# Kernel optimization log

Hardware: AMD Instinct MI355X
Metric: run time of the kernel (lower is better)

Reference implementation:

```python
import jax, jax.numpy as jnp
import numpy as np

N = 50000   # nodes
E = 800000  # edges
IN, H, OUT = 64, 512, 128


def _lin_init(key, out_dim, in_dim):
    kw, kb = jax.random.split(key)
    bound = 1.0 / np.sqrt(in_dim)
    W = jax.random.uniform(kw, (out_dim, in_dim), jnp.float32, -bound, bound)
    b = jax.random.uniform(kb, (out_dim,), jnp.float32, -bound, bound)
    return W, b


def setup_inputs() -> dict:
    key = jax.random.key(0)
    ks = jax.random.split(key, 10)
    x = jax.random.normal(ks[0], (N, IN), jnp.float32)
    edge_index = jax.random.randint(ks[1], (2, E), 0, N, jnp.int64)
    W_s1, b_s1 = _lin_init(ks[2], H, IN)
    W_s2, b_s2 = _lin_init(ks[3], H, H)
    W_s3, b_s3 = _lin_init(ks[4], H, H)
    W_s4, b_s4 = _lin_init(ks[5], H, H)
    W_m1, b_m1 = _lin_init(ks[6], OUT, H)
    W_m2, b_m2 = _lin_init(ks[7], OUT, OUT)
    W_l1, b_l1 = _lin_init(ks[8], OUT, H)
    W_l2, b_l2 = _lin_init(ks[9], OUT, OUT)
    return {"x": x, "edge_index": edge_index,
            "W_s1": W_s1, "b_s1": b_s1, "W_s2": W_s2, "b_s2": b_s2,
            "W_s3": W_s3, "b_s3": b_s3, "W_s4": W_s4, "b_s4": b_s4,
            "W_m1": W_m1, "b_m1": b_m1, "W_m2": W_m2, "b_m2": b_m2,
            "W_l1": W_l1, "b_l1": b_l1, "W_l2": W_l2, "b_l2": b_l2}


def _aggregate(h, src, dst):
    # GINConv with default eps=0: (1+eps)*x + sum_{j in N(i)} x_j
    return h + jax.ops.segment_sum(h[src], dst, num_segments=N)


def reference(x, edge_index,
              W_s1, b_s1, W_s2, b_s2, W_s3, b_s3, W_s4, b_s4,
              W_m1, b_m1, W_m2, b_m2, W_l1, b_l1, W_l2, b_l2):
    src, dst = edge_index[0], edge_index[1]
    lrelu = lambda v: jax.nn.leaky_relu(v, 0.1)

    def mlp_shared(h):
        h = lrelu(h @ W_s1.T + b_s1)
        h = lrelu(h @ W_s2.T + b_s2)
        h = lrelu(h @ W_s3.T + b_s3)
        return h @ W_s4.T + b_s4

    def mlp_mu(h):
        return jax.nn.relu(h @ W_m1.T + b_m1) @ W_m2.T + b_m2

    def mlp_logvar(h):
        return jax.nn.relu(h @ W_l1.T + b_l1) @ W_l2.T + b_l2

    h = jax.nn.relu(mlp_shared(_aggregate(x, src, dst)))
    mu = mlp_mu(_aggregate(h, src, dst))
    logvar = mlp_logvar(_aggregate(h, src, dst))
    return (mu, logvar)
```

## Files before the change

kernel.cpp:

```cpp
#include <hip/hip_runtime.h>
#include <hip/hip_bf16.h>
#include <stdint.h>

#define N_NODES 50000
#define N_PAD   50048
#define E_EDGES 800000
#define MT      391

typedef __bf16 bf16x8 __attribute__((ext_vector_type(8)));
typedef __bf16 bf16x4 __attribute__((ext_vector_type(4)));
typedef float  f32x4  __attribute__((ext_vector_type(4)));

__global__ void count_deg(const int* __restrict__ ei, int* __restrict__ cnt) {
    int e = blockIdx.x * blockDim.x + threadIdx.x;
    if (e < E_EDGES) atomicAdd(&cnt[ei[E_EDGES + e]], 1);
}

#define SCAN_B 1024
__global__ void scan_block(const int* __restrict__ cnt, int* __restrict__ ptr,
                           int* __restrict__ bsum, int n) {
    __shared__ int buf[SCAN_B];
    int i = blockIdx.x * SCAN_B + threadIdx.x;
    int v = (i < n) ? cnt[i] : 0;
    buf[threadIdx.x] = v;
    __syncthreads();
    #pragma unroll
    for (int off = 1; off < SCAN_B; off <<= 1) {
        int t = (threadIdx.x >= (unsigned)off) ? buf[threadIdx.x - off] : 0;
        __syncthreads();
        buf[threadIdx.x] += t;
        __syncthreads();
    }
    if (i < n) ptr[i] = buf[threadIdx.x] - v;
    if (threadIdx.x == SCAN_B - 1) bsum[blockIdx.x] = buf[SCAN_B - 1];
}

__global__ void scan_bsums(const int* __restrict__ bsum, int* __restrict__ boff,
                           int nb, int* __restrict__ total_out) {
    __shared__ int buf[SCAN_B];
    int v = ((int)threadIdx.x < nb) ? bsum[threadIdx.x] : 0;
    buf[threadIdx.x] = v;
    __syncthreads();
    #pragma unroll
    for (int off = 1; off < SCAN_B; off <<= 1) {
        int t = (threadIdx.x >= (unsigned)off) ? buf[threadIdx.x - off] : 0;
        __syncthreads();
        buf[threadIdx.x] += t;
        __syncthreads();
    }
    if ((int)threadIdx.x < nb) boff[threadIdx.x] = buf[threadIdx.x] - v;
    if (threadIdx.x == SCAN_B - 1) *total_out = buf[SCAN_B - 1];
}

__global__ void scan_add(int* __restrict__ ptr, const int* __restrict__ boff, int n) {
    int i = blockIdx.x * SCAN_B + threadIdx.x;
    if (i < n) ptr[i] += boff[blockIdx.x];
}

__global__ void fill_csr(const int* __restrict__ ei, const int* __restrict__ ptr,
                         int* __restrict__ cursor, int* __restrict__ col) {
    int e = blockIdx.x * blockDim.x + threadIdx.x;
    if (e < E_EDGES) {
        int dst = ei[E_EDGES + e];
        int pos = ptr[dst] + atomicAdd(&cursor[dst], 1);
        col[pos] = ei[e];
    }
}

#define XN      3200000
#define WTOT    983040
__global__ void cvt_all(const float* __restrict__ x,
                        const float* __restrict__ Ws1, const float* __restrict__ Ws2,
                        const float* __restrict__ Ws3, const float* __restrict__ Ws4,
                        const float* __restrict__ Wm1, const float* __restrict__ Wl1,
                        const float* __restrict__ Wm2, const float* __restrict__ Wl2,
                        __bf16* __restrict__ xb, __bf16* __restrict__ wbuf) {
    int i = blockIdx.x * blockDim.x + threadIdx.x;
    if (i < XN) { xb[i] = (__bf16)x[i]; return; }
    int j = i - XN;
    if (j >= WTOT) return;
    const float* s; int o;
    if      (j <  32768) { s = Ws1; o = j; }
    else if (j < 294912) { s = Ws2; o = j -  32768; }
    else if (j < 557056) { s = Ws3; o = j - 294912; }
    else if (j < 819200) { s = Ws4; o = j - 557056; }
    else if (j < 884736) { s = Wm1; o = j - 819200; }
    else if (j < 950272) { s = Wl1; o = j - 884736; }
    else if (j < 966656) { s = Wm2; o = j - 950272; }
    else                 { s = Wl2; o = j - 966656; }
    wbuf[j] = (__bf16)s[o];
}

__global__ __launch_bounds__(256) void agg0_gather(
    const __bf16* __restrict__ xb, const int* __restrict__ ptr,
    const int* __restrict__ col, __bf16* __restrict__ out) {
    int node = blockIdx.x * 4 + (threadIdx.x >> 6);
    int lane = threadIdx.x & 63;
    int g    = lane >> 3;
    int f0   = (lane & 7) << 3;
    if (node >= N_PAD) return;
    long o = (long)node * 64 + f0;
    if (node >= N_NODES) {
        if (g == 0) {
            bf16x8 z;
            #pragma unroll
            for (int i = 0; i < 8; ++i) z[i] = (__bf16)0.0f;
            *(bf16x8*)&out[o] = z;
        }
        return;
    }
    float a[8];
    #pragma unroll
    for (int i = 0; i < 8; ++i) a[i] = 0.0f;
    if (g == 0) {
        bf16x8 s = *(const bf16x8*)&xb[o];
        #pragma unroll
        for (int i = 0; i < 8; ++i) a[i] = (float)s[i];
    }
    int e0 = ptr[node], e1 = ptr[node + 1];
    int e = e0;
    for (; e + 16 <= e1; e += 16) {
        int c0 = col[e + g];
        int c1 = col[e + 8 + g];
        bf16x8 v0 = *(const bf16x8*)&xb[(c0 << 6) + f0];
        bf16x8 v1 = *(const bf16x8*)&xb[(c1 << 6) + f0];
        #pragma unroll
        for (int i = 0; i < 8; ++i) a[i] += (float)v0[i] + (float)v1[i];
    }
    int rem = e1 - e;
    if (rem > 0) {
        int u0 = (g < rem) ? g : 0;        float m0 = (g < rem) ? 1.0f : 0.0f;
        int i1 = g + 8;
        int u1 = (i1 < rem) ? i1 : 0;      float m1 = (i1 < rem) ? 1.0f : 0.0f;
        int c0 = col[e + u0];
        int c1 = col[e + u1];
        bf16x8 v0 = *(const bf16x8*)&xb[(c0 << 6) + f0];
        bf16x8 v1 = *(const bf16x8*)&xb[(c1 << 6) + f0];
        #pragma unroll
        for (int i = 0; i < 8; ++i) a[i] += m0 * (float)v0[i] + m1 * (float)v1[i];
    }
    #pragma unroll
    for (int i = 0; i < 8; ++i) {
        a[i] += __shfl_xor(a[i], 8, 64);
        a[i] += __shfl_xor(a[i], 16, 64);
        a[i] += __shfl_xor(a[i], 32, 64);
    }
    if (g == 0) {
        bf16x8 r;
        #pragma unroll
        for (int i = 0; i < 8; ++i) r[i] = (__bf16)a[i];
        *(bf16x8*)&out[o] = r;
    }
}

__global__ __launch_bounds__(256) void aggt_gather(
    const __bf16* __restrict__ t, const int* __restrict__ ptr,
    const int* __restrict__ col, const float* __restrict__ b_m1,
    const float* __restrict__ b_l1, __bf16* __restrict__ p) {
    int node = blockIdx.x * 8 + (threadIdx.x >> 5);
    if (node >= N_NODES) return;
    int hl = threadIdx.x & 31;
    int f0 = hl << 3;
    float a[8];
    {
        bf16x8 s = *(const bf16x8*)&t[((long)node << 8) + f0];
        #pragma unroll
        for (int i = 0; i < 8; ++i) a[i] = (float)s[i];
    }
    int e0 = ptr[node], e1 = ptr[node + 1];
    int e = e0;
    for (; e + 8 <= e1; e += 8) {
        int c[8];
        #pragma unroll
        for (int u = 0; u < 8; ++u) c[u] = col[e + u];
        bf16x8 v[8];
        #pragma unroll
        for (int u = 0; u < 8; ++u) v[u] = *(const bf16x8*)&t[((long)c[u] << 8) + f0];
        #pragma unroll
        for (int u = 0; u < 8; ++u)
            #pragma unroll
            for (int i = 0; i < 8; ++i) a[i] += (float)v[u][i];
    }
    int rem = e1 - e;
    if (rem > 0) {
        #pragma unroll
        for (int u = 0; u < 7; ++u) {
            int   uu = (u < rem) ? u : 0;
            float m  = (u < rem) ? 1.0f : 0.0f;
            int   cc = col[e + uu];
            bf16x8 v = *(const bf16x8*)&t[((long)cc << 8) + f0];
            #pragma unroll
            for (int i = 0; i < 8; ++i) a[i] += m * (float)v[i];
        }
    }
    const float* bp = (f0 < 128) ? (b_m1 + f0) : (b_l1 + (f0 - 128));
    f32x4 b0 = *(const f32x4*)bp;
    f32x4 b1 = *(const f32x4*)(bp + 4);
    bf16x8 r;
    #pragma unroll
    for (int i = 0; i < 4; ++i) r[i]     = (__bf16)fmaxf(a[i]     + b0[i], 0.0f);
    #pragma unroll
    for (int i = 0; i < 4; ++i) r[4 + i] = (__bf16)fmaxf(a[4 + i] + b1[i], 0.0f);
    *(bf16x8*)&p[((long)node << 8) + f0] = r;
}

__device__ __forceinline__ void gl_lds16(const __bf16* g, __bf16* l) {
    __builtin_amdgcn_global_load_lds(
        (const __attribute__((address_space(1))) uint32_t*)g,
        (__attribute__((address_space(3))) uint32_t*)l, 16, 0, 0);
}

#define P_WAITN(n) asm volatile("s_waitcnt vmcnt(" #n ")" ::: "memory")
#define P_WAIT0    asm volatile("s_waitcnt vmcnt(0)" ::: "memory")
#define P_LGKM0    asm volatile("s_waitcnt lgkmcnt(0)" ::: "memory")
#define P_BAR      __builtin_amdgcn_s_barrier()
#define SLOT_ELEMS 16384

__device__ __forceinline__ void stage_chunk(const __bf16* __restrict__ W, int Kdim,
                                            int k0, bool rows512,
                                            __bf16* __restrict__ buf,
                                            int wid, int lane) {
    if (rows512) {
        int r16 = lane >> 2, sl = lane & 3;
        #pragma unroll
        for (int i = 0; i < 4; ++i) {
            int cc = wid * 4 + i;
            int r  = cc * 16 + r16;
            int kt = sl ^ ((r >> 1) & 3);
            gl_lds16(W + (long)r * Kdim + k0 + kt * 8, buf + cc * 512);
        }
    } else {
        int r8 = lane >> 3, sl = lane & 7;
        #pragma unroll
        for (int i = 0; i < 4; ++i) {
            int cc = wid * 4 + i;
            int r  = cc * 8 + r8;
            int kt = sl ^ (r & 7);
            gl_lds16(W + (long)r * Kdim + k0 + kt * 8, buf + cc * 512);
        }
    }
}

__device__ __forceinline__ void chunk_mfma4(const __bf16* __restrict__ sAct,
    const __bf16* __restrict__ buf, int c, int rA, int q, int wncol,
    f32x4 (&acc)[4][4]) {
    const int g   = c * 4 + q;
    const int sla = ((g & 56) | ((g & 7) ^ (rA & 7))) << 3;
    bf16x8 af[4], bfr[4];
    #pragma unroll
    for (int mi = 0; mi < 4; ++mi)
        af[mi] = *(const bf16x8*)&sAct[(mi * 16 + rA) * 512 + sla];
    #pragma unroll
    for (int ni = 0; ni < 4; ++ni) {
        int wr = wncol + ni * 16 + rA;
        bfr[ni] = *(const bf16x8*)&buf[wr * 32 + ((q ^ ((wr >> 1) & 3)) << 3)];
    }
    __builtin_amdgcn_s_setprio(1);
    #pragma unroll
    for (int mi = 0; mi < 4; ++mi)
        #pragma unroll
        for (int ni = 0; ni < 4; ++ni)
            acc[mi][ni] = __builtin_amdgcn_mfma_f32_16x16x32_bf16(
                af[mi], bfr[ni], acc[mi][ni], 0, 0, 0);
    __builtin_amdgcn_s_setprio(0);
}

__device__ __forceinline__ void chunk_mfma_a0(const __bf16* __restrict__ act0,
    const __bf16* __restrict__ buf, int c, int rA, int q, int wncol,
    f32x4 (&acc)[4][4]) {
    const int g   = c * 4 + q;
    const int sla = (g ^ (rA & 7)) << 3;
    bf16x8 af[4], bfr[4];
    #pragma unroll
    for (int mi = 0; mi < 4; ++mi)
        af[mi] = *(const bf16x8*)&act0[(mi * 16 + rA) * 64 + sla];
    #pragma unroll
    for (int ni = 0; ni < 4; ++ni) {
        int wr = wncol + ni * 16 + rA;
        bfr[ni] = *(const bf16x8*)&buf[wr * 32 + ((q ^ ((wr >> 1) & 3)) << 3)];
    }
    __builtin_amdgcn_s_setprio(1);
    #pragma unroll
    for (int mi = 0; mi < 4; ++mi)
        #pragma unroll
        for (int ni = 0; ni < 4; ++ni)
            acc[mi][ni] = __builtin_amdgcn_mfma_f32_16x16x32_bf16(
                af[mi], bfr[ni], acc[mi][ni], 0, 0, 0);
    __builtin_amdgcn_s_setprio(0);
}

__device__ __forceinline__ void chunk_mfma_proj(const __bf16* __restrict__ sAct,
    const __bf16* __restrict__ buf, int c, int rA, int q, int wnp,
    f32x4 (&accp)[4][2]) {
    __builtin_amdgcn_s_setprio(1);
    #pragma unroll
    for (int s = 0; s < 2; ++s) {
        const int g   = c * 8 + s * 4 + q;
        const int sla = ((g & 56) | ((g & 7) ^ (rA & 7))) << 3;
        bf16x8 af[4], bfr[2];
        #pragma unroll
        for (int mi = 0; mi < 4; ++mi)
            af[mi] = *(const bf16x8*)&sAct[(mi * 16 + rA) * 512 + sla];
        #pragma unroll
        for (int ni = 0; ni < 2; ++ni) {
            int wr = wnp + ni * 16 + rA;
            int gB = s * 4 + q;
            bfr[ni] = *(const bf16x8*)&buf[wr * 64 + ((gB ^ (wr & 7)) << 3)];
        }
        #pragma unroll
        for (int mi = 0; mi < 4; ++mi)
            #pragma unroll
            for (int ni = 0; ni < 2; ++ni)
                accp[mi][ni] = __builtin_amdgcn_mfma_f32_16x16x32_bf16(
                    af[mi], bfr[ni], accp[mi][ni], 0, 0, 0);
    }
    __builtin_amdgcn_s_setprio(0);
}

template <int ACTn>
__device__ __forceinline__ void writeback_act(__bf16* __restrict__ sAct,
    f32x4 (&acc)[4][4], const float* __restrict__ bv,
    int wn, int ccol, int crow) {
    #pragma unroll
    for (int mi = 0; mi < 4; ++mi)
        #pragma unroll
        for (int ni = 0; ni < 4; ++ni) {
            int cc = wn + ni * 16 + ccol;
            int g  = cc >> 3;
            #pragma unroll
            for (int p = 0; p < 4; ++p) {
                int rr = mi * 16 + crow + p;
                float v = acc[mi][ni][p] + bv[ni];
                if (ACTn == 1) v = (v > 0.0f) ? v : 0.1f * v;
                else           v = fmaxf(v, 0.0f);
                int sl = (g & 56) | ((g & 7) ^ (rr & 7));
                sAct[rr * 512 + sl * 8 + (cc & 7)] = (__bf16)v;
            }
        }
}

template <int ACTn, int B3>
__device__ __forceinline__ void layer512_pipe3(
    __bf16* __restrict__ sAct, __bf16* __restrict__ sbase,
    const __bf16* __restrict__ W,
    const __bf16* __restrict__ Wn, int Kn, bool n512, int k0n_c0, int k0n_c1,
    const float* __restrict__ bv,
    int wn, int rA, int q, int ccol, int crow, int wid, int lane) {
    f32x4 acc[4][4];
    #pragma unroll
    for (int i = 0; i < 4; ++i)
        #pragma unroll
        for (int j = 0; j < 4; ++j) acc[i][j] = (f32x4)0.0f;
    #pragma unroll
    for (int c = 0; c < 16; ++c) {
        P_WAITN(4); P_BAR;
        __bf16* dst = sbase + (((B3 + c + 2) % 3) * SLOT_ELEMS);
        if (c <= 13)      stage_chunk(W, 512, (c + 2) * 32, true, dst, wid, lane);
        else if (c == 14) stage_chunk(Wn, Kn, k0n_c0, n512, dst, wid, lane);
        else              stage_chunk(Wn, Kn, k0n_c1, n512, dst, wid, lane);
        chunk_mfma4(sAct, sbase + (((B3 + c) % 3) * SLOT_ELEMS), c, rA, q, wn, acc);
    }
    P_BAR;
    writeback_act<ACTn>(sAct, acc, bv, wn, ccol, crow);
    P_LGKM0; P_BAR;
}

__global__ __launch_bounds__(512) void mlp_fused(
    const __bf16* __restrict__ a0,
    const __bf16* __restrict__ w1, const float* __restrict__ b1,
    const __bf16* __restrict__ w2, const float* __restrict__ b2,
    const __bf16* __restrict__ w3, const float* __restrict__ b3,
    const __bf16* __restrict__ w4, const float* __restrict__ b4,
    const __bf16* __restrict__ wp,
    __bf16* __restrict__ tg)
{
    __shared__ __bf16 lds[81920];
    __bf16* sAct  = lds;
    __bf16* sbase = lds + 32768;

    const int tid  = threadIdx.x;
    const int wid  = tid >> 6;
    const int lane = tid & 63;
    const long blockRow = (long)blockIdx.x * 64;

    const int rA   = lane & 15;
    const int q    = lane >> 4;
    const int ccol = lane & 15;
    const int crow = (lane >> 4) << 2;
    const int wn   = wid << 6;
    const int wnp  = wid << 5;

    float bv1[4], bv2[4], bv3[4], bv4[4];
    #pragma unroll
    for (int ni = 0; ni < 4; ++ni) {
        int idx = wn + ni * 16 + ccol;
        bv1[ni] = b1[idx]; bv2[ni] = b2[idx]; bv3[ni] = b3[idx]; bv4[ni] = b4[idx];
    }

    {
        int srow = lane >> 3;
        int skg  = (lane & 7) ^ srow;
        gl_lds16(a0 + (blockRow + wid * 8 + srow) * 64 + skg * 8, lds + wid * 512);
    }
    stage_chunk(w1, 64, 0,  true, sbase,              wid, lane);
    stage_chunk(w1, 64, 32, true, sbase + SLOT_ELEMS, wid, lane);

    {
        f32x4 acc[4][4];
        #pragma unroll
        for (int i = 0; i < 4; ++i)
            #pragma unroll
            for (int j = 0; j < 4; ++j) acc[i][j] = (f32x4)0.0f;
        P_WAIT0; P_BAR;
        stage_chunk(w2, 512, 0, true, sbase + 2 * SLOT_ELEMS, wid, lane);
        chunk_mfma_a0(lds, sbase, 0, rA, q, wn, acc);
        P_WAITN(4); P_BAR;
        stage_chunk(w2, 512, 32, true, sbase, wid, lane);
        chunk_mfma_a0(lds, sbase + SLOT_ELEMS, 1, rA, q, wn, acc);
        P_BAR;
        writeback_act<1>(sAct, acc, bv1, wn, ccol, crow);
        P_LGKM0; P_BAR;
    }

    layer512_pipe3<1, 2>(sAct, sbase, w2, w3, 512, true, 0, 32, bv2,
                         wn, rA, q, ccol, crow, wid, lane);
    layer512_pipe3<1, 0>(sAct, sbase, w3, w4, 512, true, 0, 32, bv3,
                         wn, rA, q, ccol, crow, wid, lane);
    layer512_pipe3<2, 1>(sAct, sbase, w4, wp, 512, false, 0, 64, bv4,
                         wn, rA, q, ccol, crow, wid, lane);

    {
        f32x4 accp[4][2];
        #pragma unroll
        for (int i = 0; i < 4; ++i)
            #pragma unroll
            for (int j = 0; j < 2; ++j) accp[i][j] = (f32x4)0.0f;
        #pragma unroll
        for (int c = 0; c < 8; ++c) {
            if (c == 7) { P_WAIT0; } else { P_WAITN(4); }
            P_BAR;
            if (c <= 5)
                stage_chunk(wp, 512, (c + 2) * 64, false,
                            sbase + (((4 + c) % 3) * SLOT_ELEMS), wid, lane);
            chunk_mfma_proj(sAct, sbase + (((2 + c) % 3) * SLOT_ELEMS),
                            c, rA, q, wnp, accp);
        }
        P_BAR;
        __bf16* s0 = sbase;
        #pragma unroll
        for (int mi = 0; mi < 4; ++mi)
            #pragma unroll
            for (int ni = 0; ni < 2; ++ni)
                #pragma unroll
                for (int p = 0; p < 4; ++p)
                    s0[(mi * 16 + crow + p) * 256 + wnp + ni * 16 + ccol] =
                        (__bf16)accp[mi][ni][p];
        __syncthreads();
        int rr = tid >> 3;
        int c0 = (tid & 7) << 5;
        const bf16x8* s = (const bf16x8*)&s0[rr * 256 + c0];
        __bf16* d = tg + (blockRow + rr) * 256 + c0;
        #pragma unroll
        for (int i = 0; i < 4; ++i) *(bf16x8*)(d + i * 8) = s[i];
    }
}

template <int NCOL>
__device__ __forceinline__ void swizzle_xy(int bid, int& x, int& y) {
    int grp  = bid / (8 * NCOL);
    int rem  = bid - grp * (8 * NCOL);
    int base = grp * 8;
    int width = MT - base; if (width > 8) width = 8;
    x = base + rem % width;
    y = rem / width;
}

template <int ACT, bool BIAS, bool OUT_BF16, bool MCHK>
__device__ __forceinline__ void gemm_core(
    const __bf16* __restrict__ A, int lda, const __bf16* __restrict__ W,
    const float* __restrict__ bias, void* __restrict__ Cout, int ldc,
    int K, long Mstore, long blockRow, int blockCol,
    __bf16* __restrict__ smem) {
    __bf16* As = smem;
    __bf16* Ws = smem + 8192;
    const int tid  = threadIdx.x;
    const int wid  = tid >> 6;
    const int lane = tid & 63;
    const int wm = (wid >> 1) << 6;
    const int wn = (wid & 1) << 6;

    f32x4 acc[4][4];
    #pragma unroll
    for (int i = 0; i < 4; ++i)
        #pragma unroll
        for (int j = 0; j < 4; ++j) acc[i][j] = (f32x4)0.0f;

    const int srow = lane >> 3;
    const int skg  = (lane & 7) ^ srow;
    const __bf16* gA[4]; const __bf16* gW[4];
    __bf16 *lA[4], *lW[4];
    #pragma unroll
    for (int i = 0; i < 4; ++i) {
        int c = wid * 4 + i;
        gA[i] = A + (blockRow + c * 8 + srow) * (long)lda + skg * 8;
        gW[i] = W + ((long)blockCol + c * 8 + srow) * (long)K + skg * 8;
        lA[i] = As + c * 512;
        lW[i] = Ws + c * 512;
    }

    const int rA = lane & 15;
    const int q  = lane >> 4;
    const int r7 = rA & 7;

    for (int k0 = 0; k0 < K; k0 += 64) {
        #pragma unroll
        for (int i = 0; i < 4; ++i) gl_lds16(gA[i] + k0, lA[i]);
        #pragma unroll
        for (int i = 0; i < 4; ++i) gl_lds16(gW[i] + k0, lW[i]);
        __syncthreads();

        #pragma unroll
        for (int s = 0; s < 2; ++s) {
            const int slot = ((s * 4 + q) ^ r7) * 8;
            bf16x8 af[4], bf[4];
            #pragma unroll
            for (int mi = 0; mi < 4; ++mi)
                af[mi] = *(const bf16x8*)&As[(wm + mi * 16 + rA) * 64 + slot];
            #pragma unroll
            for (int ni = 0; ni < 4; ++ni)
                bf[ni] = *(const bf16x8*)&Ws[(wn + ni * 16 + rA) * 64 + slot];
            #pragma unroll
            for (int mi = 0; mi < 4; ++mi)
                #pragma unroll
                for (int ni = 0; ni < 4; ++ni)
                    acc[mi][ni] = __builtin_amdgcn_mfma_f32_16x16x32_bf16(
                        af[mi], bf[ni], acc[mi][ni], 0, 0, 0);
        }
        __syncthreads();
    }

    const int ccol = lane & 15;
    const int crow = (lane >> 4) << 2;
    if (OUT_BF16 && !MCHK) {
        #pragma unroll
        for (int mi = 0; mi < 4; ++mi) {
            #pragma unroll
            for (int ni = 0; ni < 4; ++ni) {
                int gc = wn + ni * 16 + ccol;
                float bv = BIAS ? bias[blockCol + gc] : 0.0f;
                #pragma unroll
                for (int r = 0; r < 4; ++r) {
                    float v = acc[mi][ni][r] + bv;
                    if (ACT == 1) v = (v > 0.0f) ? v : 0.1f * v;
                    else if (ACT == 2) v = fmaxf(v, 0.0f);
                    smem[(wm + mi * 16 + crow + r) * 128 + gc] = (__bf16)v;
                }
            }
        }
        __syncthreads();
        #pragma unroll
        for (int i = 0; i < 8; ++i) {
            int o   = (i * 256 + tid) * 8;
            int row = o >> 7;
            int co  = o & 127;
            *(bf16x8*)((__bf16*)Cout + (blockRow + row) * (long)ldc + blockCol + co) =
                *(const bf16x8*)&smem[o];
        }
    } else if (!OUT_BF16) {
        float* fsmem = (float*)smem;
        #pragma unroll
        for (int half = 0; half < 2; ++half) {
            __syncthreads();
            if ((wm >> 6) == half) {
                #pragma unroll
                for (int mi = 0; mi < 4; ++mi) {
                    #pragma unroll
                    for (int ni = 0; ni < 4; ++ni) {
                        int gc = wn + ni * 16 + ccol;
                        float bv = BIAS ? bias[blockCol + gc] : 0.0f;
                        #pragma unroll
                        for (int r = 0; r < 4; ++r) {
                            float v = acc[mi][ni][r] + bv;
                            if (ACT == 1) v = (v > 0.0f) ? v : 0.1f * v;
                            else if (ACT == 2) v = fmaxf(v, 0.0f);
                            fsmem[(mi * 16 + crow + r) * 128 + gc] = v;
                        }
                    }
                }
            }
            __syncthreads();
            #pragma unroll
            for (int i = 0; i < 8; ++i) {
                int o   = i * 256 + tid;
                int row = o >> 5;
                int co  = (o & 31) * 4;
                long gr = blockRow + half * 64 + row;
                if (!MCHK || gr < Mstore)
                    *(f32x4*)((float*)Cout + gr * (long)ldc + blockCol + co) =
                        *(const f32x4*)&fsmem[o * 4];
            }
        }
    } else {
        #pragma unroll
        for (int mi = 0; mi < 4; ++mi) {
            #pragma unroll
            for (int ni = 0; ni < 4; ++ni) {
                long gr0 = blockRow + wm + mi * 16 + crow;
                int  gc  = blockCol + wn + ni * 16 + ccol;
                float bv = BIAS ? bias[gc] : 0.0f;
                #pragma unroll
                for (int r = 0; r < 4; ++r) {
                    long gr = gr0 + r;
                    if (!MCHK || gr < Mstore) {
                        float v = acc[mi][ni][r] + bv;
                        if (ACT == 1) v = (v > 0.0f) ? v : 0.1f * v;
                        else if (ACT == 2) v = fmaxf(v, 0.0f);
                        ((__bf16*)Cout)[gr * ldc + gc] = (__bf16)v;
                    }
                }
            }
        }
    }
}

__global__ __launch_bounds__(256) void gemm_heads(
    const __bf16* __restrict__ p, const __bf16* __restrict__ wm2,
    const float* __restrict__ b_m2, float* __restrict__ mu,
    const __bf16* __restrict__ wl2, const float* __restrict__ b_l2,
    float* __restrict__ lv) {
    __shared__ __bf16 smem[128 * 128];
    int x, hd;
    swizzle_xy<2>(blockIdx.x, x, hd);
    if (hd == 0)
        gemm_core<0, true, false, true>(p, 256, wm2, b_m2, mu, 128, 128, N_NODES,
                                        (long)x * 128, 0, smem);
    else
        gemm_core<0, true, false, true>(p + 128, 256, wl2, b_l2, lv, 128, 128, N_NODES,
                                        (long)x * 128, 0, smem);
}

extern "C" void kernel_launch(void* const* d_in, const int* in_sizes, int n_in,
                              void* d_out, int out_size, void* d_ws, size_t ws_size,
                              hipStream_t stream) {
    const float* x    = (const float*)d_in[0];
    const int*   ei   = (const int*)d_in[1];
    const float* W_s1 = (const float*)d_in[2];
    const float* b_s1 = (const float*)d_in[3];
    const float* W_s2 = (const float*)d_in[4];
    const float* b_s2 = (const float*)d_in[5];
    const float* W_s3 = (const float*)d_in[6];
    const float* b_s3 = (const float*)d_in[7];
    const float* W_s4 = (const float*)d_in[8];
    const float* b_s4 = (const float*)d_in[9];
    const float* W_m1 = (const float*)d_in[10];
    const float* b_m1 = (const float*)d_in[11];
    const float* W_m2 = (const float*)d_in[12];
    const float* b_m2 = (const float*)d_in[13];
    const float* W_l1 = (const float*)d_in[14];
    const float* b_l1 = (const float*)d_in[15];
    const float* W_l2 = (const float*)d_in[16];
    const float* b_l2 = (const float*)d_in[17];

    char* ws = (char*)d_ws;
    size_t off = 0;
    auto carve = [&](size_t bytes) -> void* {
        void* p = ws + off;
        off = (off + bytes + 255) & ~(size_t)255;
        return p;
    };
    int* ptr  = (int*)carve((size_t)(N_NODES + 1) * 4);
    int* col  = (int*)carve((size_t)E_EDGES * 4);
    int* bsum = (int*)carve(SCAN_B * 4);
    int* boff = (int*)carve(SCAN_B * 4);
    __bf16* wbuf = (__bf16*)carve((size_t)WTOT * 2);
    __bf16* w1  = wbuf;
    __bf16* w2  = wbuf +  32768;
    __bf16* w3  = wbuf + 294912;
    __bf16* w4  = wbuf + 557056;
    __bf16* wml = wbuf + 819200;
    __bf16* wm2 = wbuf + 950272;
    __bf16* wl2 = wbuf + 966656;
    __bf16* xb    = (__bf16*)carve((size_t)XN * 2);
    __bf16* agg0b = (__bf16*)carve((size_t)N_PAD * 64 * 2);
    __bf16* B1    = (__bf16*)carve((size_t)N_PAD * 512 * 2);
    __bf16* B2    = (__bf16*)carve((size_t)N_PAD * 512 * 2);

    int* cnt = (int*)B1;
    int* cur = (int*)B2;

    (void)hipMemsetAsync(cnt, 0, (size_t)N_NODES * 4, stream);
    (void)hipMemsetAsync(cur, 0, (size_t)N_NODES * 4, stream);

    const int NB = (N_NODES + SCAN_B - 1) / SCAN_B;
    count_deg<<<E_EDGES / 256, 256, 0, stream>>>(ei, cnt);
    scan_block<<<NB, SCAN_B, 0, stream>>>(cnt, ptr, bsum, N_NODES);
    scan_bsums<<<1, SCAN_B, 0, stream>>>(bsum, boff, NB, &ptr[N_NODES]);
    scan_add<<<NB, SCAN_B, 0, stream>>>(ptr, boff, N_NODES);
    fill_csr<<<E_EDGES / 256, 256, 0, stream>>>(ei, ptr, cur, col);

    cvt_all<<<(XN + WTOT + 255) / 256, 256, 0, stream>>>(
        x, W_s1, W_s2, W_s3, W_s4, W_m1, W_l1, W_m2, W_l2, xb, wbuf);

    agg0_gather<<<N_PAD / 4, 256, 0, stream>>>(xb, ptr, col, agg0b);

    __bf16* t = B1;
    mlp_fused<<<N_PAD / 64, 512, 0, stream>>>(agg0b, w1, b_s1, w2, b_s2,
                                              w3, b_s3, w4, b_s4, wml, t);

    __bf16* p = B2;
    aggt_gather<<<(N_NODES + 7) / 8, 256, 0, stream>>>(t, ptr, col, b_m1, b_l1, p);

    float* mu = (float*)d_out;
    float* lv = mu + (size_t)N_NODES * 128;
    gemm_heads<<<MT * 2, 256, 0, stream>>>(p, wm2, b_m2, mu, wl2, b_l2, lv);
}
```

Measured before the change: 443.4 us.

## Give each wave private weight double-buffers and fuse degree counting into conversion kernel

The fused MLP kernel switches from block-shared triple-buffered weight chunks staged by all waves (with a barrier per chunk) to per-wave private double buffers. Each wave stages only the 64 weight rows (32 for the projection) it consumes, so the per-chunk block barriers can be dropped. Sched barriers replace setprio, and LDS usage shrinks, which could allow higher occupancy. Separately, the degree-count atomics are merged into the fp32-to-bf16 conversion kernel, removing one launch. The risk is less cross-wave sharing of staged data and weaker latency hiding with only two buffers.

```diff
diff --git a/kernel.cpp b/kernel.cpp
--- a/kernel.cpp
+++ b/kernel.cpp
@@ -10,11 +10,6 @@
 typedef __bf16 bf16x8 __attribute__((ext_vector_type(8)));
 typedef __bf16 bf16x4 __attribute__((ext_vector_type(4)));
 typedef float  f32x4  __attribute__((ext_vector_type(4)));
-
-__global__ void count_deg(const int* __restrict__ ei, int* __restrict__ cnt) {
-    int e = blockIdx.x * blockDim.x + threadIdx.x;
-    if (e < E_EDGES) atomicAdd(&cnt[ei[E_EDGES + e]], 1);
-}
 
 #define SCAN_B 1024
 __global__ void scan_block(const int* __restrict__ cnt, int* __restrict__ ptr,
@@ -69,26 +64,32 @@
 
 #define XN      3200000
 #define WTOT    983040
-__global__ void cvt_all(const float* __restrict__ x,
-                        const float* __restrict__ Ws1, const float* __restrict__ Ws2,
-                        const float* __restrict__ Ws3, const float* __restrict__ Ws4,
-                        const float* __restrict__ Wm1, const float* __restrict__ Wl1,
-                        const float* __restrict__ Wm2, const float* __restrict__ Wl2,
-                        __bf16* __restrict__ xb, __bf16* __restrict__ wbuf) {
+__global__ void cvt_count(const float* __restrict__ x,
+                          const float* __restrict__ Ws1, const float* __restrict__ Ws2,
+                          const float* __restrict__ Ws3, const float* __restrict__ Ws4,
+                          const float* __restrict__ Wm1, const float* __restrict__ Wl1,
+                          const float* __restrict__ Wm2, const float* __restrict__ Wl2,
+                          const int* __restrict__ ei,
+                          __bf16* __restrict__ xb, __bf16* __restrict__ wbuf,
+                          int* __restrict__ cnt) {
     int i = blockIdx.x * blockDim.x + threadIdx.x;
     if (i < XN) { xb[i] = (__bf16)x[i]; return; }
     int j = i - XN;
-    if (j >= WTOT) return;
-    const float* s; int o;
-    if      (j <  32768) { s = Ws1; o = j; }
-    else if (j < 294912) { s = Ws2; o = j -  32768; }
-    else if (j < 557056) { s = Ws3; o = j - 294912; }
-    else if (j < 819200) { s = Ws4; o = j - 557056; }
-    else if (j < 884736) { s = Wm1; o = j - 819200; }
-    else if (j < 950272) { s = Wl1; o = j - 884736; }
-    else if (j < 966656) { s = Wm2; o = j - 950272; }
-    else                 { s = Wl2; o = j - 966656; }
-    wbuf[j] = (__bf16)s[o];
+    if (j < WTOT) {
+        const float* s; int o;
+        if      (j <  32768) { s = Ws1; o = j; }
+        else if (j < 294912) { s = Ws2; o = j -  32768; }
+        else if (j < 557056) { s = Ws3; o = j - 294912; }
+        else if (j < 819200) { s = Ws4; o = j - 557056; }
+        else if (j < 884736) { s = Wm1; o = j - 819200; }
+        else if (j < 950272) { s = Wl1; o = j - 884736; }
+        else if (j < 966656) { s = Wm2; o = j - 950272; }
+        else                 { s = Wl2; o = j - 966656; }
+        wbuf[j] = (__bf16)s[o];
+        return;
+    }
+    int e = j - WTOT;
+    if (e < E_EDGES) atomicAdd(&cnt[ei[E_EDGES + e]], 1);
 }
 
 __global__ __launch_bounds__(256) void agg0_gather(
@@ -214,35 +215,35 @@
 #define P_WAIT0    asm volatile("s_waitcnt vmcnt(0)" ::: "memory")
 #define P_LGKM0    asm volatile("s_waitcnt lgkmcnt(0)" ::: "memory")
 #define P_BAR      __builtin_amdgcn_s_barrier()
-#define SLOT_ELEMS 16384
-
-__device__ __forceinline__ void stage_chunk(const __bf16* __restrict__ W, int Kdim,
-                                            int k0, bool rows512,
-                                            __bf16* __restrict__ buf,
-                                            int wid, int lane) {
-    if (rows512) {
-        int r16 = lane >> 2, sl = lane & 3;
-        #pragma unroll
-        for (int i = 0; i < 4; ++i) {
-            int cc = wid * 4 + i;
-            int r  = cc * 16 + r16;
-            int kt = sl ^ ((r >> 1) & 3);
-            gl_lds16(W + (long)r * Kdim + k0 + kt * 8, buf + cc * 512);
-        }
-    } else {
-        int r8 = lane >> 3, sl = lane & 7;
-        #pragma unroll
-        for (int i = 0; i < 4; ++i) {
-            int cc = wid * 4 + i;
-            int r  = cc * 8 + r8;
-            int kt = sl ^ (r & 7);
-            gl_lds16(W + (long)r * Kdim + k0 + kt * 8, buf + cc * 512);
-        }
-    }
-}
-
-__device__ __forceinline__ void chunk_mfma4(const __bf16* __restrict__ sAct,
-    const __bf16* __restrict__ buf, int c, int rA, int q, int wncol,
+#define P_SGB      __builtin_amdgcn_sched_barrier(0)
+#define SLOTE      2048
+
+__device__ __forceinline__ void stage_w64(const __bf16* __restrict__ W, int Kdim,
+                                          int k0, int wn,
+                                          __bf16* __restrict__ slot, int lane) {
+    int r16 = lane >> 2, sl = lane & 3;
+    #pragma unroll
+    for (int i = 0; i < 4; ++i) {
+        int rl = i * 16 + r16;
+        int kt = sl ^ ((rl >> 1) & 3);
+        gl_lds16(W + (long)(wn + rl) * Kdim + k0 + kt * 8, slot + i * 512);
+    }
+}
+
+__device__ __forceinline__ void stage_wp32(const __bf16* __restrict__ W, int k0,
+                                           int wnp, __bf16* __restrict__ slot,
+                                           int lane) {
+    int r8 = lane >> 3, sl = lane & 7;
+    #pragma unroll
+    for (int i = 0; i < 4; ++i) {
+        int rl = i * 8 + r8;
+        int kt = sl ^ (rl & 7);
+        gl_lds16(W + (long)(wnp + rl) * 512 + k0 + kt * 8, slot + i * 512);
+    }
+}
+
+__device__ __forceinline__ void chunk_mfma4L(const __bf16* __restrict__ sAct,
+    const __bf16* __restrict__ buf, int c, int rA, int q,
     f32x4 (&acc)[4][4]) {
     const int g   = c * 4 + q;
     const int sla = ((g & 56) | ((g & 7) ^ (rA & 7))) << 3;
@@ -252,21 +253,19 @@
         af[mi] = *(const bf16x8*)&sAct[(mi * 16 + rA) * 512 + sla];
     #pragma unroll
     for (int ni = 0; ni < 4; ++ni) {
-        int wr = wncol + ni * 16 + rA;
-        bfr[ni] = *(const bf16x8*)&buf[wr * 32 + ((q ^ ((wr >> 1) & 3)) << 3)];
-    }
-    __builtin_amdgcn_s_setprio(1);
+        int wrl = ni * 16 + rA;
+        bfr[ni] = *(const bf16x8*)&buf[wrl * 32 + ((q ^ ((wrl >> 1) & 3)) << 3)];
+    }
     #pragma unroll
     for (int mi = 0; mi < 4; ++mi)
         #pragma unroll
         for (int ni = 0; ni < 4; ++ni)
             acc[mi][ni] = __builtin_amdgcn_mfma_f32_16x16x32_bf16(
                 af[mi], bfr[ni], acc[mi][ni], 0, 0, 0);
-    __builtin_amdgcn_s_setprio(0);
-}
-
-__device__ __forceinline__ void chunk_mfma_a0(const __bf16* __restrict__ act0,
-    const __bf16* __restrict__ buf, int c, int rA, int q, int wncol,
+}
+
+__device__ __forceinline__ void chunk_mfma_a0L(const __bf16* __restrict__ act0,
+    const __bf16* __restrict__ buf, int c, int rA, int q,
     f32x4 (&acc)[4][4]) {
     const int g   = c * 4 + q;
     const int sla = (g ^ (rA & 7)) << 3;
@@ -276,23 +275,20 @@
         af[mi] = *(const bf16x8*)&act0[(mi * 16 + rA) * 64 + sla];
     #pragma unroll
     for (int ni = 0; ni < 4; ++ni) {
-        int wr = wncol + ni * 16 + rA;
-        bfr[ni] = *(const bf16x8*)&buf[wr * 32 + ((q ^ ((wr >> 1) & 3)) << 3)];
-    }
-    __builtin_amdgcn_s_setprio(1);
+        int wrl = ni * 16 + rA;
+        bfr[ni] = *(const bf16x8*)&buf[wrl * 32 + ((q ^ ((wrl >> 1) & 3)) << 3)];
+    }
     #pragma unroll
     for (int mi = 0; mi < 4; ++mi)
         #pragma unroll
         for (int ni = 0; ni < 4; ++ni)
             acc[mi][ni] = __builtin_amdgcn_mfma_f32_16x16x32_bf16(
                 af[mi], bfr[ni], acc[mi][ni], 0, 0, 0);
-    __builtin_amdgcn_s_setprio(0);
-}
-
-__device__ __forceinline__ void chunk_mfma_proj(const __bf16* __restrict__ sAct,
-    const __bf16* __restrict__ buf, int c, int rA, int q, int wnp,
+}
+
+__device__ __forceinline__ void chunk_mfma_projL(const __bf16* __restrict__ sAct,
+    const __bf16* __restrict__ buf, int c, int rA, int q,
     f32x4 (&accp)[4][2]) {
-    __builtin_amdgcn_s_setprio(1);
     #pragma unroll
     for (int s = 0; s < 2; ++s) {
         const int g   = c * 8 + s * 4 + q;
@@ -303,9 +299,9 @@
             af[mi] = *(const bf16x8*)&sAct[(mi * 16 + rA) * 512 + sla];
         #pragma unroll
         for (int ni = 0; ni < 2; ++ni) {
-            int wr = wnp + ni * 16 + rA;
-            int gB = s * 4 + q;
-            bfr[ni] = *(const bf16x8*)&buf[wr * 64 + ((gB ^ (wr & 7)) << 3)];
+            int wrl = ni * 16 + rA;
+            int gB  = s * 4 + q;
+            bfr[ni] = *(const bf16x8*)&buf[wrl * 64 + ((gB ^ (wrl & 7)) << 3)];
         }
         #pragma unroll
         for (int mi = 0; mi < 4; ++mi)
@@ -314,7 +310,6 @@
                 accp[mi][ni] = __builtin_amdgcn_mfma_f32_16x16x32_bf16(
                     af[mi], bfr[ni], accp[mi][ni], 0, 0, 0);
     }
-    __builtin_amdgcn_s_setprio(0);
 }
 
 template <int ACTn>
@@ -339,13 +334,12 @@
         }
 }
 
-template <int ACTn, int B3>
-__device__ __forceinline__ void layer512_pipe3(
-    __bf16* __restrict__ sAct, __bf16* __restrict__ sbase,
-    const __bf16* __restrict__ W,
-    const __bf16* __restrict__ Wn, int Kn, bool n512, int k0n_c0, int k0n_c1,
+template <int ACTn, bool NPROJ>
+__device__ __forceinline__ void layer512_wv(
+    __bf16* __restrict__ sAct, __bf16* __restrict__ sA, __bf16* __restrict__ sB,
+    const __bf16* __restrict__ W, const __bf16* __restrict__ Wn,
     const float* __restrict__ bv,
-    int wn, int rA, int q, int ccol, int crow, int wid, int lane) {
+    int wn, int wnp, int rA, int q, int ccol, int crow, int lane) {
     f32x4 acc[4][4];
     #pragma unroll
     for (int i = 0; i < 4; ++i)
@@ -353,12 +347,13 @@
         for (int j = 0; j < 4; ++j) acc[i][j] = (f32x4)0.0f;
     #pragma unroll
     for (int c = 0; c < 16; ++c) {
-        P_WAITN(4); P_BAR;
-        __bf16* dst = sbase + (((B3 + c + 2) % 3) * SLOT_ELEMS);
-        if (c <= 13)      stage_chunk(W, 512, (c + 2) * 32, true, dst, wid, lane);
-        else if (c == 14) stage_chunk(Wn, Kn, k0n_c0, n512, dst, wid, lane);
-        else              stage_chunk(Wn, Kn, k0n_c1, n512, dst, wid, lane);
-        chunk_mfma4(sAct, sbase + (((B3 + c) % 3) * SLOT_ELEMS), c, rA, q, wn, acc);
+        P_WAITN(4);
+        __bf16* cur = (c & 1) ? sB : sA;
+        chunk_mfma4L(sAct, cur, c, rA, q, acc);
+        P_SGB;
+        if (c <= 13)      stage_w64(W, 512, (c + 2) * 32, wn, cur, lane);
+        else if (!NPROJ)  stage_w64(Wn, 512, (c - 14) * 32, wn, cur, lane);
+        else              stage_wp32(Wn, (c - 14) * 64, wnp, cur, lane);
     }
     P_BAR;
     writeback_act<ACTn>(sAct, acc, bv, wn, ccol, crow);
@@ -374,9 +369,10 @@
     const __bf16* __restrict__ wp,
     __bf16* __restrict__ tg)
 {
-    __shared__ __bf16 lds[81920];
-    __bf16* sAct  = lds;
-    __bf16* sbase = lds + 32768;
+    __shared__ __bf16 lds[69632];
+    __bf16* act0  = lds;
+    __bf16* sAct  = lds + 4096;
+    __bf16* slots = lds + 36864;
 
     const int tid  = threadIdx.x;
     const int wid  = tid >> 6;
@@ -390,6 +386,16 @@
     const int wn   = wid << 6;
     const int wnp  = wid << 5;
 
+    __bf16* sA = slots + (wid * 2) * SLOTE;
+    __bf16* sB = sA + SLOTE;
+
+    {
+        int srow = lane >> 3;
+        int skg  = (lane & 7) ^ srow;
+        gl_lds16(a0 + (blockRow + wid * 8 + srow) * 64 + skg * 8, act0 + wid * 512);
+    }
+    stage_w64(w1, 64, 0,  wn, sA, lane);
+    stage_w64(w1, 64, 32, wn, sB, lane);
     float bv1[4], bv2[4], bv3[4], bv4[4];
     #pragma unroll
     for (int ni = 0; ni < 4; ++ni) {
@@ -397,13 +403,8 @@
         bv1[ni] = b1[idx]; bv2[ni] = b2[idx]; bv3[ni] = b3[idx]; bv4[ni] = b4[idx];
     }
 
-    {
-        int srow = lane >> 3;
-        int skg  = (lane & 7) ^ srow;
-        gl_lds16(a0 + (blockRow + wid * 8 + srow) * 64 + skg * 8, lds + wid * 512);
-    }
-    stage_chunk(w1, 64, 0,  true, sbase,              wid, lane);
-    stage_chunk(w1, 64, 32, true, sbase + SLOT_ELEMS, wid, lane);
+    asm volatile("s_waitcnt vmcnt(0) lgkmcnt(0)" ::: "memory");
+    P_BAR;
 
     {
         f32x4 acc[4][4];
@@ -411,23 +412,21 @@
         for (int i = 0; i < 4; ++i)
             #pragma unroll
             for (int j = 0; j < 4; ++j) acc[i][j] = (f32x4)0.0f;
-        P_WAIT0; P_BAR;
-        stage_chunk(w2, 512, 0, true, sbase + 2 * SLOT_ELEMS, wid, lane);
-        chunk_mfma_a0(lds, sbase, 0, rA, q, wn, acc);
-        P_WAITN(4); P_BAR;
-        stage_chunk(w2, 512, 32, true, sbase, wid, lane);
-        chunk_mfma_a0(lds, sbase + SLOT_ELEMS, 1, rA, q, wn, acc);
+        chunk_mfma_a0L(act0, sA, 0, rA, q, acc);
+        P_SGB;
+        stage_w64(w2, 512, 0, wn, sA, lane);
+        P_WAITN(4);
+        chunk_mfma_a0L(act0, sB, 1, rA, q, acc);
+        P_SGB;
+        stage_w64(w2, 512, 32, wn, sB, lane);
         P_BAR;
         writeback_act<1>(sAct, acc, bv1, wn, ccol, crow);
         P_LGKM0; P_BAR;
     }
 
-    layer512_pipe3<1, 2>(sAct, sbase, w2, w3, 512, true, 0, 32, bv2,
-                         wn, rA, q, ccol, crow, wid, lane);
-    layer512_pipe3<1, 0>(sAct, sbase, w3, w4, 512, true, 0, 32, bv3,
-                         wn, rA, q, ccol, crow, wid, lane);
-    layer512_pipe3<2, 1>(sAct, sbase, w4, wp, 512, false, 0, 64, bv4,
-                         wn, rA, q, ccol, crow, wid, lane);
+    layer512_wv<1, false>(sAct, sA, sB, w2, w3, bv2, wn, wnp, rA, q, ccol, crow, lane);
+    layer512_wv<1, false>(sAct, sA, sB, w3, w4, bv3, wn, wnp, rA, q, ccol, crow, lane);
+    layer512_wv<2, true >(sAct, sA, sB, w4, wp, bv4, wn, wnp, rA, q, ccol, crow, lane);
 
     {
         f32x4 accp[4][2];
@@ -438,15 +437,13 @@
         #pragma unroll
         for (int c = 0; c < 8; ++c) {
             if (c == 7) { P_WAIT0; } else { P_WAITN(4); }
-            P_BAR;
-            if (c <= 5)
-                stage_chunk(wp, 512, (c + 2) * 64, false,
-                            sbase + (((4 + c) % 3) * SLOT_ELEMS), wid, lane);
-            chunk_mfma_proj(sAct, sbase + (((2 + c) % 3) * SLOT_ELEMS),
-                            c, rA, q, wnp, accp);
+            __bf16* cur = (c & 1) ? sB : sA;
+            chunk_mfma_projL(sAct, cur, c, rA, q, accp);
+            P_SGB;
+            if (c <= 5) stage_wp32(wp, (c + 2) * 64, wnp, cur, lane);
         }
         P_BAR;
-        __bf16* s0 = sbase;
+        __bf16* s0 = slots;
         #pragma unroll
         for (int mi = 0; mi < 4; ++mi)
             #pragma unroll
@@ -691,16 +688,15 @@
     (void)hipMemsetAsync(cnt, 0, (size_t)N_NODES * 4, stream);
     (void)hipMemsetAsync(cur, 0, (size_t)N_NODES * 4, stream);
 
+    cvt_count<<<(XN + WTOT + E_EDGES + 255) / 256, 256, 0, stream>>>(
+        x, W_s1, W_s2, W_s3, W_s4, W_m1, W_l1, W_m2, W_l2, ei, xb, wbuf, cnt);
+
     const int NB = (N_NODES + SCAN_B - 1) / SCAN_B;
-    count_deg<<<E_EDGES / 256, 256, 0, stream>>>(ei, cnt);
     scan_block<<<NB, SCAN_B, 0, stream>>>(cnt, ptr, bsum, N_NODES);
     scan_bsums<<<1, SCAN_B, 0, stream>>>(bsum, boff, NB, &ptr[N_NODES]);
     scan_add<<<NB, SCAN_B, 0, stream>>>(ptr, boff, N_NODES);
     fill_csr<<<E_EDGES / 256, 256, 0, stream>>>(ei, ptr, cur, col);
 
-    cvt_all<<<(XN + WTOT + 255) / 256, 256, 0, stream>>>(
-        x, W_s1, W_s2, W_s3, W_s4, W_m1, W_l1, W_m2, W_l2, xb, wbuf);
-
     agg0_gather<<<N_PAD / 4, 256, 0, stream>>>(xb, ptr, col, agg0b);
 
     __bf16* t = B1;
```

Result: faster. 426.0 us (median of 2 runs) (-3.9%).
